# Kernel optimization log

Hardware: AMD Instinct MI355X
Metric: run time of the kernel (lower is better)

## Reference

```python
import jax, jax.numpy as jnp
import numpy as np

B, T_PAST, T_FUT, GH, GW = 256, 20, 30, 100, 100
HID = 32  # past_encoder_dim


def gru_cell(x, h, w_ih, w_hh, b_ih, b_hh):
    # torch nn.GRU single-cell math; weights [3H, in], [3H, H]
    gi = x @ w_ih.T + b_ih
    gh = h @ w_hh.T + b_hh
    i_r, i_z, i_n = jnp.split(gi, 3, axis=-1)
    h_r, h_z, h_n = jnp.split(gh, 3, axis=-1)
    r = jax.nn.sigmoid(i_r + h_r)
    zg = jax.nn.sigmoid(i_z + h_z)
    n = jnp.tanh(i_n + r * h_n)
    return (1.0 - zg) * n + zg * h


def bilinear(grid, q):
    # grid [B,H,W,C]; q [B,2], dim 0 -> height, dim 1 -> width (matches torch code)
    Bn, Hh, Ww, C = grid.shape
    fy = jnp.clip(jnp.floor(q[:, 0]), 0.0, Hh - 2).astype(jnp.int32)
    fx = jnp.clip(jnp.floor(q[:, 1]), 0.0, Ww - 2).astype(jnp.int32)
    ay = jnp.clip(q[:, 0] - fy, 0.0, 1.0)[:, None]
    ax = jnp.clip(q[:, 1] - fx, 0.0, 1.0)[:, None]
    b = jnp.arange(Bn)
    tl = grid[b, fy, fx]
    tr = grid[b, fy, fx + 1]
    bl = grid[b, fy + 1, fx]
    br = grid[b, fy + 1, fx + 1]
    top = tl + ax * (tr - tl)
    bot = bl + ax * (br - bl)
    return top + ay * (bot - top)  # [B,C]


def setup_inputs() -> dict:
    key = jax.random.key(0)
    ks = jax.random.split(key, 24)
    s = 0.05
    f32 = jnp.float32
    inp = {
        'z': jax.random.normal(ks[0], (B, T_FUT, 2), f32),
        'player_past': jax.random.uniform(ks[1], (B, T_PAST, 2), f32) * (GH - 10),
        'lidar': jax.random.normal(ks[2], (B, GH, GW, 2), f32),
        'conv0_w': jax.random.normal(ks[3], (2, 2, 2, 32), f32) * s,   # HWIO
        'conv0_b': jnp.zeros((32,), f32),
        'conv1_w': jax.random.normal(ks[4], (2, 2, 32, 32), f32) * s,
        'conv1_b': jnp.zeros((32,), f32),
        'conv2_w': jax.random.normal(ks[5], (2, 2, 32, 32), f32) * s,
        'conv2_b': jnp.zeros((32,), f32),
        'conv3_w': jax.random.normal(ks[6], (2, 2, 32, 32), f32) * s,
        'conv3_b': jnp.zeros((32,), f32),
        'enc_wih': jax.random.normal(ks[7], (3 * HID, 2), f32) * s,
        'enc_whh': jax.random.normal(ks[8], (3 * HID, HID), f32) * s,
        'enc_bih': jnp.zeros((3 * HID,), f32),
        'enc_bhh': jnp.zeros((3 * HID,), f32),
        'dec_wih': jax.random.normal(ks[9], (3 * HID, HID + 2), f32) * s,
        'dec_whh': jax.random.normal(ks[10], (3 * HID, HID), f32) * s,
        'dec_bih': jnp.zeros((3 * HID,), f32),
        'dec_bhh': jnp.zeros((3 * HID,), f32),
        'mlp_w1': jax.random.normal(ks[11], (512, HID), f32) * s,
        'mlp_b1': jnp.zeros((512,), f32),
        'mlp_w2': jax.random.normal(ks[12], (4, 512), f32) * s,
        'mlp_b2': jnp.zeros((4,), f32),
    }
    return inp


def reference(z, player_past, lidar,
              conv0_w, conv0_b, conv1_w, conv1_b, conv2_w, conv2_b, conv3_w, conv3_b,
              enc_wih, enc_whh, enc_bih, enc_bhh,
              dec_wih, dec_whh, dec_bih, dec_bhh,
              mlp_w1, mlp_b1, mlp_w2, mlp_b2):
    # field model: ZeroPad2d((0,1,0,1)) + Conv 2x2 + ReLU, x4 -> same-size NHWC conv
    v = lidar
    for w, b in ((conv0_w, conv0_b), (conv1_w, conv1_b), (conv2_w, conv2_b), (conv3_w, conv3_b)):
        v = jax.nn.relu(jax.lax.conv_general_dilated(
            v, w, (1, 1), [(0, 1), (0, 1)],
            dimension_numbers=('NHWC', 'HWIO', 'NHWC')) + b)
    context_lidar = v  # [B,GH,GW,32]

    # past encoder GRU; last output of single-layer GRU == final hidden
    h0 = jnp.zeros((z.shape[0], HID), z.dtype)
    def enc_step(h, x_t):
        return gru_cell(x_t, h, enc_wih, enc_whh, enc_bih, enc_bhh), None
    h_enc, _ = jax.lax.scan(enc_step, h0, jnp.swapaxes(player_past, 0, 1))

    y_tm2 = player_past[:, -2, :]
    y_tm1 = player_past[:, -1, :]

    def dec_step(carry, z_t):
        h, y1, y2 = carry
        interp_t = bilinear(context_lidar, y1)                 # [B,32]
        x = jnp.concatenate([y1, interp_t], axis=-1)            # [B,34]
        h = gru_cell(x, h, dec_wih, dec_whh, dec_bih, dec_bhh)
        # locscale_mlp: Linear(32,512) -> Linear(512,4) (no ReLU between, per source)
        ls = (h @ mlp_w1.T + mlp_b1) @ mlp_w2.T + mlp_b2
        loc = ls[:, :2]
        scale = jax.nn.softplus(ls[:, 2:])
        y_t = 2.0 * y1 - y2 + loc + scale * z_t                 # verlet + affine sample
        return (h, y_t, y1), (y_t, scale)

    _, (ys, scales) = jax.lax.scan(dec_step, (h_enc, y_tm1, y_tm2), jnp.swapaxes(z, 0, 1))
    y = jnp.swapaxes(ys, 0, 1)          # [B,T,2]
    scales = jnp.swapaxes(scales, 0, 1)  # [B,T,2]
    logabsdet = jnp.sum(jnp.log(jnp.abs(jnp.prod(scales, axis=-2))), axis=-1)  # [B]
    return (y, logabsdet)
```

## Files before the change

### kernel.cpp

```cpp
#include <hip/hip_runtime.h>
#include <math.h>

typedef __attribute__((ext_vector_type(8))) short    short8;
typedef __attribute__((ext_vector_type(4))) float    f32x4;
typedef __attribute__((ext_vector_type(4))) unsigned uint4v;

#define FRAG0 256

__device__ __forceinline__ unsigned short f2bf(float f) {
    unsigned u = __builtin_bit_cast(unsigned, f);
    u = u + 0x7fffu + ((u >> 16) & 1u);
    return (unsigned short)(u >> 16);
}
__device__ __forceinline__ unsigned packRNE(float hi, float lo) {
    return (unsigned)f2bf(lo) | ((unsigned)f2bf(hi) << 16);
}
__device__ __forceinline__ unsigned pack_trunc(float hi, float lo) {
    return __builtin_amdgcn_perm(__builtin_bit_cast(unsigned, hi),
                                 __builtin_bit_cast(unsigned, lo), 0x07060302u);
}
__device__ __forceinline__ float rfl(float x) {
    return __builtin_bit_cast(float, __builtin_amdgcn_readfirstlane(__builtin_bit_cast(int, x)));
}
__device__ __forceinline__ f32x4 mfma16(short8 a, short8 b, f32x4 c) {
    return __builtin_amdgcn_mfma_f32_16x16x32_bf16(a, b, c, 0, 0, 0);
}
__device__ __forceinline__ unsigned bperm(int addr, unsigned v) {
    return (unsigned)__builtin_amdgcn_ds_bpermute(addr, (int)v);
}
template<int PAT>
__device__ __forceinline__ float swzXf(float v) {
    return __builtin_bit_cast(float, __builtin_amdgcn_ds_swizzle(__builtin_bit_cast(int, v), PAT));
}
__device__ __forceinline__ unsigned swz1u(unsigned v){ return (unsigned)__builtin_amdgcn_ds_swizzle((int)v, 0x041F); }
__device__ __forceinline__ float sigf(float x) { return __builtin_amdgcn_rcpf(1.f + __expf(-x)); }
__device__ __forceinline__ float tanhfast(float x) {
    float e = __expf(2.f * x);
    return 1.f - 2.f * __builtin_amdgcn_rcpf(e + 1.f);
}
__device__ __forceinline__ f32x4 ld4(const float* p) { return *(const f32x4*)p; }

__device__ __forceinline__ void packC(unsigned* P, f32x4 a0, f32x4 a1, bool oob) {
    float r0 = fmaxf(a0[0], 0.f), r1 = fmaxf(a0[1], 0.f), r2 = fmaxf(a0[2], 0.f), r3 = fmaxf(a0[3], 0.f);
    float s0 = fmaxf(a1[0], 0.f), s1 = fmaxf(a1[1], 0.f), s2 = fmaxf(a1[2], 0.f), s3 = fmaxf(a1[3], 0.f);
    P[0] = pack_trunc(r1, r0); P[1] = pack_trunc(r3, r2);
    P[2] = pack_trunc(s1, s0); P[3] = pack_trunc(s3, s2);
    if (oob) { P[0] = 0u; P[1] = 0u; P[2] = 0u; P[3] = 0u; }
}

__global__ __launch_bounds__(256) void r2p2_prep(
    const float* __restrict__ w0, const float* __restrict__ w1,
    const float* __restrict__ w2, const float* __restrict__ w3,
    const float* __restrict__ enc_whh,
    const float* __restrict__ dec_wih, const float* __restrict__ dec_whh,
    const float* __restrict__ mw1, const float* __restrict__ mb1,
    const float* __restrict__ mw2, const float* __restrict__ mb2,
    float* __restrict__ wsf, unsigned* __restrict__ wsu) {
    const int tid = threadIdx.x, bx = blockIdx.x;
    if (bx == 0) {
        __shared__ float red[64];
        if (tid < 128) {
            int k = tid & 31, j = tid >> 5;
            const float* w2r = mw2 + j * 512;
            float a0 = 0.f, a1 = 0.f, a2 = 0.f, a3 = 0.f;
#pragma unroll 4
            for (int m = 0; m < 512; m += 4) {
                a0 = fmaf(w2r[m],     mw1[m * 32 + k],       a0);
                a1 = fmaf(w2r[m + 1], mw1[(m + 1) * 32 + k], a1);
                a2 = fmaf(w2r[m + 2], mw1[(m + 2) * 32 + k], a2);
                a3 = fmaf(w2r[m + 3], mw1[(m + 3) * 32 + k], a3);
            }
            wsf[j * 32 + k] = (a0 + a1) + (a2 + a3);
        } else if (tid < 192) {
            int t = tid - 128;
            int j = t & 3, ch = t >> 2;
            const float* w2c = mw2 + j * 512 + ch * 32;
            const float* b1c = mb1 + ch * 32;
            float p = 0.f;
#pragma unroll 8
            for (int m = 0; m < 32; ++m) p = fmaf(w2c[m], b1c[m], p);
            red[t] = p;
        }
        __syncthreads();
        if (tid < 4) {
            float c = mb2[tid];
#pragma unroll
            for (int i = 0; i < 16; ++i) c += red[tid + i * 4];
            wsf[128 + tid] = c;
        }
        return;
    }
    int base = (bx - 1) * 416;
    for (int c = base + tid; c < base + 416 && c < 2816; c += 256) {
        int f = c >> 6, lane = c & 63;
        int n = lane & 15, q = lane >> 4;
        int pc0 = ((n >> 2) << 3) | (n & 3);
        float v[8];
        if (f < 2) {
            int co = pc0 + f * 4;
#pragma unroll
            for (int j = 0; j < 8; ++j) v[j] = (q == 0) ? w0[j * 32 + co] : 0.f;
        } else if (f < 26) {
            int t = f - 2;
            const float* W = (t < 8) ? w1 : (t < 16) ? w2 : w3;
            t &= 7;
            int mt = t >> 2, ks = t & 3, co = pc0 + mt * 4;
#pragma unroll
            for (int j = 0; j < 8; ++j) v[j] = W[(ks * 32 + q * 8 + j) * 32 + co];
        } else if (f < 32) {
            int t = f - 26, gate = t >> 1, mt = t & 1;
            int row = gate * 32 + pc0 + mt * 4;
#pragma unroll
            for (int j = 0; j < 8; ++j) v[j] = dec_wih[row * 34 + 2 + q * 8 + j];
        } else if (f < 38) {
            int t = f - 32, gate = t >> 1, mt = t & 1;
            int row = gate * 32 + pc0 + mt * 4;
#pragma unroll
            for (int j = 0; j < 8; ++j) v[j] = dec_whh[row * 32 + q * 8 + j];
        } else {
            int t = f - 38, gate = t >> 1, mt = t & 1;
            int row = gate * 32 + pc0 + mt * 4;
#pragma unroll
            for (int j = 0; j < 8; ++j) v[j] = enc_whh[row * 32 + q * 8 + j];
        }
        uint4v u;
        u[0] = packRNE(v[1], v[0]); u[1] = packRNE(v[3], v[2]);
        u[2] = packRNE(v[5], v[4]); u[3] = packRNE(v[7], v[6]);
        *(uint4v*)(wsu + FRAG0 + f * 256 + lane * 4) = u;
    }
}

__global__ __launch_bounds__(256)
void r2p2_main(
    const float* __restrict__ z, const float* __restrict__ past, const float* __restrict__ lidar,
    const float* __restrict__ b0, const float* __restrict__ b1,
    const float* __restrict__ b2, const float* __restrict__ b3,
    const float* __restrict__ enc_wih, const float* __restrict__ enc_bih, const float* __restrict__ enc_bhh,
    const float* __restrict__ dec_wih, const float* __restrict__ dec_bih, const float* __restrict__ dec_bhh,
    const float* __restrict__ wsf, const unsigned* __restrict__ wsu,
    float* __restrict__ out) {

    const int tid = threadIdx.x, b = blockIdx.x;
    const int wid = tid >> 6, lane = tid & 63;
    const int n = lane & 15, q = lane >> 4, e = n & 1;

    __shared__ __align__(16) unsigned sLID[104 * 104];
    __shared__ __align__(16) float PASTs[40];
    __shared__ __align__(16) float ZVs[64];

    if (wid != 0) {
        int st = tid - 64;
        if (st < 60) ZVs[st] = z[b * 60 + st];
        for (int i = st; i < 816; i += 192) {
            int idx = (i < 416) ? (10400 + i) : ((((i - 416) >> 2) * 104) + 100 + ((i - 416) & 3));
            sLID[idx] = 0u;
        }
        const float4* lp4 = (const float4*)(lidar + (size_t)b * 20000);
#pragma unroll 4
        for (int i = st; i < 5000; i += 192) {
            int r = (int)(((unsigned)i * 5243u) >> 18);
            int c2 = i - r * 50;
            float4 v = lp4[i];
            int o = r * 104 + 2 * c2;
            sLID[o]     = pack_trunc(v.y, v.x);
            sLID[o + 1] = pack_trunc(v.w, v.z);
        }
        __syncthreads();
        return;
    }

    uint4v FR[44];
#pragma unroll
    for (int f = 0; f < 44; ++f) FR[f] = *(const uint4v*)(wsu + FRAG0 + f * 256 + lane * 4);
#define FRG(f) __builtin_bit_cast(short8, FR[f])

    f32x4 cb0[2], cb1[2], cb2[2], cb3[2], gbR[2], gbZ[2], gbNi[2], gbNh[2];
    f32x4 egR[2], egZ[2], egNh[2];
#pragma unroll
    for (int mt = 0; mt < 2; ++mt) {
        int o = q * 8 + mt * 4;
        cb0[mt] = ld4(b0 + o); cb1[mt] = ld4(b1 + o); cb2[mt] = ld4(b2 + o); cb3[mt] = ld4(b3 + o);
        gbR[mt]  = ld4(dec_bih + o)      + ld4(dec_bhh + o);
        gbZ[mt]  = ld4(dec_bih + 32 + o) + ld4(dec_bhh + 32 + o);
        gbNi[mt] = ld4(dec_bih + 64 + o);
        gbNh[mt] = ld4(dec_bhh + 64 + o);
        egR[mt]  = ld4(enc_bih + o)      + ld4(enc_bhh + o);
        egZ[mt]  = ld4(enc_bih + 32 + o) + ld4(enc_bhh + 32 + o);
        egNh[mt] = ld4(enc_bhh + 64 + o);
    }
    f32x4 ebni = ld4(enc_bih + 64 + q * 8 + e * 4);
    float2 wxr[4], wxz[4], wxn[4], wexr[4], wexz[4], wexn[4];
#pragma unroll
    for (int r = 0; r < 4; ++r) {
        int c = q * 8 + e * 4 + r;
        wxr[r]  = *(const float2*)(dec_wih + c * 34);
        wxz[r]  = *(const float2*)(dec_wih + (32 + c) * 34);
        wxn[r]  = *(const float2*)(dec_wih + (64 + c) * 34);
        wexr[r] = *(const float2*)(enc_wih + c * 2);
        wexz[r] = *(const float2*)(enc_wih + (32 + c) * 2);
        wexn[r] = *(const float2*)(enc_wih + (64 + c) * 2);
    }
    short8 Am = (short8)0;
    if (n < 4) {
#pragma unroll
        for (int j = 0; j < 8; ++j) Am[j] = (short)f2bf(wsf[n * 32 + q * 8 + j]);
    }
    f32x4 mcv = {0.f, 0.f, 0.f, 0.f};
    if (q == 0) mcv = *(const f32x4*)(wsf + 128);

    if (lane < 20) *(float2*)&PASTs[2 * lane] = *(const float2*)(past + b * 40 + 2 * lane);
    float q0 = past[b * 40 + 38], q1 = past[b * 40 + 39];
    float p0 = past[b * 40 + 36], p1 = past[b * 40 + 37];
    asm volatile("s_waitcnt lgkmcnt(0)" ::: "memory");

    float hq[4] = {0.f, 0.f, 0.f, 0.f};
    short8 hfr = (short8)0;
#pragma unroll 1
    for (int t = 0; t < 20; ++t) {
        float2 xp = *(const float2*)&PASTs[2 * t];
        f32x4 gr0 = mfma16(FRG(38), hfr, egR[0]),  gr1 = mfma16(FRG(39), hfr, egR[1]);
        f32x4 gz0 = mfma16(FRG(40), hfr, egZ[0]),  gz1 = mfma16(FRG(41), hfr, egZ[1]);
        f32x4 gh0 = mfma16(FRG(42), hfr, egNh[0]), gh1 = mfma16(FRG(43), hfr, egNh[1]);
        f32x4 grS = e ? gr1 : gr0, gzS = e ? gz1 : gz0, ghS = e ? gh1 : gh0;
        float hn[4];
#pragma unroll
        for (int r = 0; r < 4; ++r) {
            float rp = grS[r] + xp.x * wexr[r].x + xp.y * wexr[r].y;
            float zp = gzS[r] + xp.x * wexz[r].x + xp.y * wexz[r].y;
            float pi = ebni[r] + xp.x * wexn[r].x + xp.y * wexn[r].y;
            float rr = sigf(rp), zz = sigf(zp);
            float tn = tanhfast(fmaf(rr, ghS[r], pi));
            float hv = tn + zz * (hq[r] - tn);
            hq[r] = hv; hn[r] = hv;
        }
        unsigned hu0 = packRNE(hn[1], hn[0]), hu1 = packRNE(hn[3], hn[2]);
        unsigned po0 = swz1u(hu0), po1 = swz1u(hu1);
        uint4v hv4;
        hv4[0] = e ? po0 : hu0; hv4[1] = e ? po1 : hu1;
        hv4[2] = e ? hu0 : po0; hv4[3] = e ? hu1 : po1;
        hfr = __builtin_bit_cast(short8, hv4);
    }

    __syncthreads();

    int py0a = n / 5, px0a = n % 5;
    int pe0b = (16 + n < 25) ? 16 + n : 24;
    int py0b = pe0b / 5, px0b = pe0b - py0b * 5;
    int ofs0a[4], ofs0b[4];
#pragma unroll
    for (int tp = 0; tp < 4; ++tp) {
        ofs0a[tp] = (py0a + (tp >> 1)) * 104 + px0a + (tp & 1);
        ofs0b[tp] = (py0b + (tp >> 1)) * 104 + px0b + (tp & 1);
    }
    int py1 = n >> 2, px1 = n & 3;
    int adr1[4], sel1m[4];
#pragma unroll
    for (int ks = 0; ks < 4; ++ks) {
        int p = (py1 + (ks >> 1)) * 5 + px1 + (ks & 1);
        adr1[ks] = (q * 16 + (p & 15)) * 4;
        sel1m[ks] = (p >= 16);
    }
    int pe2 = (n < 9) ? n : 8, py2 = pe2 / 3, px2 = pe2 - py2 * 3;
    int adr2[4];
#pragma unroll
    for (int ks = 0; ks < 4; ++ks) adr2[ks] = (q * 16 + (py2 + (ks >> 1)) * 4 + px2 + (ks & 1)) * 4;
    int pe3 = n & 3, py3 = pe3 >> 1, px3 = pe3 & 1;
    int adr3[4];
#pragma unroll
    for (int ks = 0; ks < 4; ++ks) adr3[ks] = (q * 16 + (py3 + (ks >> 1)) * 3 + px3 + (ks & 1)) * 4;
    const f32x4 zf4 = {0.f, 0.f, 0.f, 0.f};
    float la = 0.f;

#pragma unroll 1
    for (int t = 0; t < 30; ++t) {
        float2 zv = *(const float2*)&ZVs[2 * t];
        float f0 = fminf(fmaxf(floorf(q0), 0.f), 98.f);
        float f1v = fminf(fmaxf(floorf(q1), 0.f), 98.f);
        int fy = (int)f0, fx = (int)f1v;
        float ay = fminf(fmaxf(q0 - f0, 0.f), 1.f);
        float ax = fminf(fmaxf(q1 - f1v, 0.f), 1.f);
        int base = fy * 104 + fx;
        int limy = 100 - fy, limx = 100 - fx;

        short8 bfa = (short8)0, bfb = (short8)0;
        if (q == 0) {
            uint4v ua, ub;
#pragma unroll
            for (int tp = 0; tp < 4; ++tp) { ua[tp] = sLID[base + ofs0a[tp]]; ub[tp] = sLID[base + ofs0b[tp]]; }
            bfa = __builtin_bit_cast(short8, ua);
            bfb = __builtin_bit_cast(short8, ub);
        }
        f32x4 ca0 = mfma16(FRG(0), bfa, cb0[0]);
        f32x4 ca1 = mfma16(FRG(1), bfa, cb0[1]);
        f32x4 cB0 = mfma16(FRG(0), bfb, cb0[0]);
        f32x4 cB1 = mfma16(FRG(1), bfb, cb0[1]);
        unsigned Pa[4], Pb[4];
        packC(Pa, ca0, ca1, (py0a >= limy) || (px0a >= limx));
        packC(Pb, cB0, cB1, (py0b >= limy) || (px0b >= limx));

        short8 bf1[4];
#pragma unroll
        for (int ks = 0; ks < 4; ++ks) {
            uint4v bu;
#pragma unroll
            for (int u = 0; u < 4; ++u) {
                unsigned va = bperm(adr1[ks], Pa[u]);
                unsigned vb = bperm(adr1[ks], Pb[u]);
                bu[u] = sel1m[ks] ? vb : va;
            }
            bf1[ks] = __builtin_bit_cast(short8, bu);
        }
        {
            f32x4 aA = mfma16(FRG(2), bf1[0], cb1[0]); aA = mfma16(FRG(3), bf1[1], aA);
            f32x4 aB = mfma16(FRG(4), bf1[2], zf4);    aB = mfma16(FRG(5), bf1[3], aB);
            f32x4 bA = mfma16(FRG(6), bf1[0], cb1[1]); bA = mfma16(FRG(7), bf1[1], bA);
            f32x4 bB = mfma16(FRG(8), bf1[2], zf4);    bB = mfma16(FRG(9), bf1[3], bB);
            f32x4 o0 = aA + aB, o1 = bA + bB;
            packC(Pa, o0, o1, (py1 >= limy) || (px1 >= limx));
        }

        short8 bf2v[4];
#pragma unroll
        for (int ks = 0; ks < 4; ++ks) {
            uint4v bu;
#pragma unroll
            for (int u = 0; u < 4; ++u) bu[u] = bperm(adr2[ks], Pa[u]);
            bf2v[ks] = __builtin_bit_cast(short8, bu);
        }
        {
            f32x4 aA = mfma16(FRG(10), bf2v[0], cb2[0]); aA = mfma16(FRG(11), bf2v[1], aA);
            f32x4 aB = mfma16(FRG(12), bf2v[2], zf4);    aB = mfma16(FRG(13), bf2v[3], aB);
            f32x4 bA = mfma16(FRG(14), bf2v[0], cb2[1]); bA = mfma16(FRG(15), bf2v[1], bA);
            f32x4 bB = mfma16(FRG(16), bf2v[2], zf4);    bB = mfma16(FRG(17), bf2v[3], bB);
            f32x4 o0 = aA + aB, o1 = bA + bB;
            packC(Pb, o0, o1, (py2 >= limy) || (px2 >= limx));
        }

        short8 bf3v[4];
#pragma unroll
        for (int ks = 0; ks < 4; ++ks) {
            uint4v bu;
#pragma unroll
            for (int u = 0; u < 4; ++u) bu[u] = bperm(adr3[ks], Pb[u]);
            bf3v[ks] = __builtin_bit_cast(short8, bu);
        }
        short8 xf;
        {
            f32x4 aA = mfma16(FRG(18), bf3v[0], cb3[0]); aA = mfma16(FRG(19), bf3v[1], aA);
            f32x4 aB = mfma16(FRG(20), bf3v[2], zf4);    aB = mfma16(FRG(21), bf3v[3], aB);
            f32x4 bA = mfma16(FRG(22), bf3v[0], cb3[1]); bA = mfma16(FRG(23), bf3v[1], bA);
            f32x4 bB = mfma16(FRG(24), bf3v[2], zf4);    bB = mfma16(FRG(25), bf3v[3], bB);
            f32x4 o0 = aA + aB, o1 = bA + bB;
            float wy = (n & 2) ? ay : 1.f - ay;
            float wx = (n & 1) ? ax : 1.f - ax;
            float w = wy * wx;
            float t0[4], t1[4];
#pragma unroll
            for (int r = 0; r < 4; ++r) { t0[r] = fmaxf(o0[r], 0.f) * w; t1[r] = fmaxf(o1[r], 0.f) * w; }
#pragma unroll
            for (int r = 0; r < 4; ++r) {
                float a1 = swzXf<0x041F>(t0[r]), a2 = swzXf<0x081F>(t0[r]), a3 = swzXf<0x0C1F>(t0[r]);
                t0[r] = (t0[r] + a1) + (a2 + a3);
                float b1v = swzXf<0x041F>(t1[r]), b2v = swzXf<0x081F>(t1[r]), b3v = swzXf<0x0C1F>(t1[r]);
                t1[r] = (t1[r] + b1v) + (b2v + b3v);
            }
            uint4v xu;
            xu[0] = packRNE(t0[1], t0[0]); xu[1] = packRNE(t0[3], t0[2]);
            xu[2] = packRNE(t1[1], t1[0]); xu[3] = packRNE(t1[3], t1[2]);
            xf = __builtin_bit_cast(short8, xu);
        }

        f32x4 gr0 = mfma16(FRG(26), xf, gbR[0]); gr0 = mfma16(FRG(32), hfr, gr0);
        f32x4 gr1 = mfma16(FRG(27), xf, gbR[1]); gr1 = mfma16(FRG(33), hfr, gr1);
        f32x4 gz0 = mfma16(FRG(28), xf, gbZ[0]); gz0 = mfma16(FRG(34), hfr, gz0);
        f32x4 gz1 = mfma16(FRG(29), xf, gbZ[1]); gz1 = mfma16(FRG(35), hfr, gz1);
        f32x4 gi0 = mfma16(FRG(30), xf, gbNi[0]);
        f32x4 gi1 = mfma16(FRG(31), xf, gbNi[1]);
        f32x4 gh0 = mfma16(FRG(36), hfr, gbNh[0]);
        f32x4 gh1 = mfma16(FRG(37), hfr, gbNh[1]);
        f32x4 grS = e ? gr1 : gr0, gzS = e ? gz1 : gz0, giS = e ? gi1 : gi0, ghS = e ? gh1 : gh0;
        float hn[4];
#pragma unroll
        for (int r = 0; r < 4; ++r) {
            float rp = grS[r] + q0 * wxr[r].x + q1 * wxr[r].y;
            float zp = gzS[r] + q0 * wxz[r].x + q1 * wxz[r].y;
            float pi = giS[r] + q0 * wxn[r].x + q1 * wxn[r].y;
            float rr = sigf(rp), zz = sigf(zp);
            float tn = tanhfast(fmaf(rr, ghS[r], pi));
            float hv = tn + zz * (hq[r] - tn);
            hq[r] = hv; hn[r] = hv;
        }
        unsigned hu0 = packRNE(hn[1], hn[0]), hu1 = packRNE(hn[3], hn[2]);
        unsigned po0 = swz1u(hu0), po1 = swz1u(hu1);
        uint4v hv4;
        hv4[0] = e ? po0 : hu0; hv4[1] = e ? po1 : hu1;
        hv4[2] = e ? hu0 : po0; hv4[3] = e ? hu1 : po1;
        hfr = __builtin_bit_cast(short8, hv4);

        f32x4 ls = mfma16(Am, hfr, mcv);
        float l2 = ls[2], l3 = ls[3];
        float s0 = fmaxf(l2, 0.f) + __logf(1.f + __expf(-fabsf(l2)));
        float s1 = fmaxf(l3, 0.f) + __logf(1.f + __expf(-fabsf(l3)));
        float ny0 = 2.f * q0 - p0 + ls[0] + s0 * zv.x;
        float ny1 = 2.f * q1 - p1 + ls[1] + s1 * zv.y;
        if (lane == 0) {
            float2 o2 = {ny0, ny1};
            *(float2*)(out + b * 60 + 2 * t) = o2;
        }
        la += __logf(s0 * s1);
        p0 = q0; p1 = q1;
        q0 = rfl(ny0); q1 = rfl(ny1);
    }
    if (lane == 0) out[15360 + b] = la;
#undef FRG
}

extern "C" void kernel_launch(void* const* d_in, const int* in_sizes, int n_in,
                              void* d_out, int out_size, void* d_ws, size_t ws_size,
                              hipStream_t stream) {
    const float* z    = (const float*)d_in[0];
    const float* past = (const float*)d_in[1];
    const float* lid  = (const float*)d_in[2];
    const float* c0w = (const float*)d_in[3];  const float* c0b = (const float*)d_in[4];
    const float* c1w = (const float*)d_in[5];  const float* c1b = (const float*)d_in[6];
    const float* c2w = (const float*)d_in[7];  const float* c2b = (const float*)d_in[8];
    const float* c3w = (const float*)d_in[9];  const float* c3b = (const float*)d_in[10];
    const float* ewih = (const float*)d_in[11]; const float* ewhh = (const float*)d_in[12];
    const float* ebih = (const float*)d_in[13]; const float* ebhh = (const float*)d_in[14];
    const float* dwih = (const float*)d_in[15]; const float* dwhh = (const float*)d_in[16];
    const float* dbih = (const float*)d_in[17]; const float* dbhh = (const float*)d_in[18];
    const float* mw1 = (const float*)d_in[19]; const float* mb1 = (const float*)d_in[20];
    const float* mw2 = (const float*)d_in[21]; const float* mb2 = (const float*)d_in[22];
    float* out = (float*)d_out;
    float* wsf = (float*)d_ws;
    unsigned* wsu = (unsigned*)d_ws;

    r2p2_prep<<<8, 256, 0, stream>>>(c0w, c1w, c2w, c3w, ewhh, dwih, dwhh,
                                     mw1, mb1, mw2, mb2, wsf, wsu);
    r2p2_main<<<256, 256, 0, stream>>>(z, past, lid, c0b, c1b, c2b, c3b,
                                       ewih, ebih, ebhh, dwih, dbih, dbhh,
                                       wsf, wsu, out);
}
```

Baseline: 182.4 us.

## Fuse weight-prep kernel into main kernel, packing fragments via shared memory

```diff
diff --git a/kernel.cpp b/kernel.cpp
--- a/kernel.cpp
+++ b/kernel.cpp
@@ -4,8 +4,6 @@
 typedef __attribute__((ext_vector_type(8))) short    short8;
 typedef __attribute__((ext_vector_type(4))) float    f32x4;
 typedef __attribute__((ext_vector_type(4))) unsigned uint4v;
-
-#define FRAG0 256
 
 __device__ __forceinline__ unsigned short f2bf(float f) {
     unsigned u = __builtin_bit_cast(unsigned, f);
@@ -48,107 +46,153 @@
     if (oob) { P[0] = 0u; P[1] = 0u; P[2] = 0u; P[3] = 0u; }
 }
 
-__global__ __launch_bounds__(256) void r2p2_prep(
-    const float* __restrict__ w0, const float* __restrict__ w1,
-    const float* __restrict__ w2, const float* __restrict__ w3,
-    const float* __restrict__ enc_whh,
-    const float* __restrict__ dec_wih, const float* __restrict__ dec_whh,
-    const float* __restrict__ mw1, const float* __restrict__ mb1,
-    const float* __restrict__ mw2, const float* __restrict__ mb2,
-    float* __restrict__ wsf, unsigned* __restrict__ wsu) {
-    const int tid = threadIdx.x, bx = blockIdx.x;
-    if (bx == 0) {
-        __shared__ float red[64];
-        if (tid < 128) {
-            int k = tid & 31, j = tid >> 5;
-            const float* w2r = mw2 + j * 512;
-            float a0 = 0.f, a1 = 0.f, a2 = 0.f, a3 = 0.f;
-#pragma unroll 4
-            for (int m = 0; m < 512; m += 4) {
-                a0 = fmaf(w2r[m],     mw1[m * 32 + k],       a0);
-                a1 = fmaf(w2r[m + 1], mw1[(m + 1) * 32 + k], a1);
-                a2 = fmaf(w2r[m + 2], mw1[(m + 2) * 32 + k], a2);
-                a3 = fmaf(w2r[m + 3], mw1[(m + 3) * 32 + k], a3);
-            }
-            wsf[j * 32 + k] = (a0 + a1) + (a2 + a3);
-        } else if (tid < 192) {
-            int t = tid - 128;
-            int j = t & 3, ch = t >> 2;
-            const float* w2c = mw2 + j * 512 + ch * 32;
-            const float* b1c = mb1 + ch * 32;
-            float p = 0.f;
-#pragma unroll 8
-            for (int m = 0; m < 32; ++m) p = fmaf(w2c[m], b1c[m], p);
-            red[t] = p;
-        }
-        __syncthreads();
-        if (tid < 4) {
-            float c = mb2[tid];
-#pragma unroll
-            for (int i = 0; i < 16; ++i) c += red[tid + i * 4];
-            wsf[128 + tid] = c;
-        }
-        return;
-    }
-    int base = (bx - 1) * 416;
-    for (int c = base + tid; c < base + 416 && c < 2816; c += 256) {
-        int f = c >> 6, lane = c & 63;
-        int n = lane & 15, q = lane >> 4;
-        int pc0 = ((n >> 2) << 3) | (n & 3);
-        float v[8];
-        if (f < 2) {
-            int co = pc0 + f * 4;
-#pragma unroll
-            for (int j = 0; j < 8; ++j) v[j] = (q == 0) ? w0[j * 32 + co] : 0.f;
-        } else if (f < 26) {
-            int t = f - 2;
-            const float* W = (t < 8) ? w1 : (t < 16) ? w2 : w3;
-            t &= 7;
-            int mt = t >> 2, ks = t & 3, co = pc0 + mt * 4;
-#pragma unroll
-            for (int j = 0; j < 8; ++j) v[j] = W[(ks * 32 + q * 8 + j) * 32 + co];
-        } else if (f < 32) {
-            int t = f - 26, gate = t >> 1, mt = t & 1;
-            int row = gate * 32 + pc0 + mt * 4;
-#pragma unroll
-            for (int j = 0; j < 8; ++j) v[j] = dec_wih[row * 34 + 2 + q * 8 + j];
-        } else if (f < 38) {
-            int t = f - 32, gate = t >> 1, mt = t & 1;
-            int row = gate * 32 + pc0 + mt * 4;
-#pragma unroll
-            for (int j = 0; j < 8; ++j) v[j] = dec_whh[row * 32 + q * 8 + j];
-        } else {
-            int t = f - 38, gate = t >> 1, mt = t & 1;
-            int row = gate * 32 + pc0 + mt * 4;
-#pragma unroll
-            for (int j = 0; j < 8; ++j) v[j] = enc_whh[row * 32 + q * 8 + j];
-        }
-        uint4v u;
-        u[0] = packRNE(v[1], v[0]); u[1] = packRNE(v[3], v[2]);
-        u[2] = packRNE(v[5], v[4]); u[3] = packRNE(v[7], v[6]);
-        *(uint4v*)(wsu + FRAG0 + f * 256 + lane * 4) = u;
-    }
+__device__ __forceinline__ uint4v ld4u(const short* p) {
+    const unsigned* u = (const unsigned*)p;
+    uint4v r; r[0] = u[0]; r[1] = u[1]; r[2] = u[2]; r[3] = u[3];
+    return r;
 }
 
 __global__ __launch_bounds__(256)
 void r2p2_main(
     const float* __restrict__ z, const float* __restrict__ past, const float* __restrict__ lidar,
-    const float* __restrict__ b0, const float* __restrict__ b1,
-    const float* __restrict__ b2, const float* __restrict__ b3,
-    const float* __restrict__ enc_wih, const float* __restrict__ enc_bih, const float* __restrict__ enc_bhh,
-    const float* __restrict__ dec_wih, const float* __restrict__ dec_bih, const float* __restrict__ dec_bhh,
-    const float* __restrict__ wsf, const unsigned* __restrict__ wsu,
+    const float* __restrict__ w0, const float* __restrict__ b0,
+    const float* __restrict__ w1, const float* __restrict__ b1,
+    const float* __restrict__ w2, const float* __restrict__ b2,
+    const float* __restrict__ w3, const float* __restrict__ b3,
+    const float* __restrict__ enc_wih, const float* __restrict__ enc_whh,
+    const float* __restrict__ enc_bih, const float* __restrict__ enc_bhh,
+    const float* __restrict__ dec_wih, const float* __restrict__ dec_whh,
+    const float* __restrict__ dec_bih, const float* __restrict__ dec_bhh,
+    const float* __restrict__ mw1, const float* __restrict__ mb1,
+    const float* __restrict__ mw2, const float* __restrict__ mb2,
     float* __restrict__ out) {
 
     const int tid = threadIdx.x, b = blockIdx.x;
     const int wid = tid >> 6, lane = tid & 63;
     const int n = lane & 15, q = lane >> 4, e = n & 1;
-
-    __shared__ __align__(16) unsigned sLID[104 * 104];
+    const int pc0 = ((n >> 2) << 3) | (n & 3);
+
+    __shared__ __align__(16) unsigned sLID[10816];
+    __shared__ __align__(16) short sG[9792];
     __shared__ __align__(16) float PASTs[40];
     __shared__ __align__(16) float ZVs[64];
-
-    if (wid != 0) {
+    __shared__ __align__(16) float MMs[132];
+
+    short* sW = (short*)sLID;
+
+    for (int i = tid; i < 4096; i += 256) {
+        int k = i >> 5, co = i & 31;
+        sW[          co * 130 + k] = (short)f2bf(w1[i]);
+        sW[4160 +    co * 130 + k] = (short)f2bf(w2[i]);
+        sW[8320 +    co * 130 + k] = (short)f2bf(w3[i]);
+    }
+    for (int i = tid; i < 3072; i += 256) {
+        int o = i >> 5, k = i & 31;
+        sG[       o * 34 + k] = (short)f2bf(dec_wih[o * 34 + 2 + k]);
+        sG[3264 + o * 34 + k] = (short)f2bf(dec_whh[i]);
+        sG[6528 + o * 34 + k] = (short)f2bf(enc_whh[i]);
+    }
+    __syncthreads();
+
+    uint4v FR[44];
+    f32x4 cb0[2], cb1[2], cb2[2], cb3[2], gbR[2], gbZ[2], gbNi[2], gbNh[2];
+    f32x4 egR[2], egZ[2], egNh[2], ebni = {0.f, 0.f, 0.f, 0.f};
+    float2 wxr[4], wxz[4], wxn[4], wexr[4], wexz[4], wexn[4];
+    float q0 = 0.f, q1 = 0.f, p0 = 0.f, p1 = 0.f;
+
+    if (wid == 0) {
+        if (q == 0) {
+#pragma unroll
+            for (int mt = 0; mt < 2; ++mt) {
+                int co = pc0 + mt * 4;
+                uint4v u;
+#pragma unroll
+                for (int i = 0; i < 4; ++i) u[i] = packRNE(w0[(2 * i + 1) * 32 + co], w0[2 * i * 32 + co]);
+                FR[mt] = u;
+            }
+        } else { FR[0] = (uint4v)0u; FR[1] = (uint4v)0u; }
+#pragma unroll
+        for (int mt = 0; mt < 2; ++mt) {
+            int co = pc0 + mt * 4;
+#pragma unroll
+            for (int ks = 0; ks < 4; ++ks) {
+                FR[ 2 + mt * 4 + ks] = ld4u(sW +        co * 130 + ks * 32 + q * 8);
+                FR[10 + mt * 4 + ks] = ld4u(sW + 4160 + co * 130 + ks * 32 + q * 8);
+                FR[18 + mt * 4 + ks] = ld4u(sW + 8320 + co * 130 + ks * 32 + q * 8);
+            }
+        }
+#pragma unroll
+        for (int g = 0; g < 3; ++g) {
+#pragma unroll
+            for (int mt = 0; mt < 2; ++mt) {
+                int o = (g * 32 + pc0 + mt * 4) * 34 + q * 8;
+                FR[26 + g * 2 + mt] = ld4u(sG + o);
+                FR[32 + g * 2 + mt] = ld4u(sG + 3264 + o);
+                FR[38 + g * 2 + mt] = ld4u(sG + 6528 + o);
+            }
+        }
+#pragma unroll
+        for (int mt = 0; mt < 2; ++mt) {
+            int o = q * 8 + mt * 4;
+            cb0[mt] = ld4(b0 + o); cb1[mt] = ld4(b1 + o); cb2[mt] = ld4(b2 + o); cb3[mt] = ld4(b3 + o);
+            gbR[mt]  = ld4(dec_bih + o)      + ld4(dec_bhh + o);
+            gbZ[mt]  = ld4(dec_bih + 32 + o) + ld4(dec_bhh + 32 + o);
+            gbNi[mt] = ld4(dec_bih + 64 + o);
+            gbNh[mt] = ld4(dec_bhh + 64 + o);
+            egR[mt]  = ld4(enc_bih + o)      + ld4(enc_bhh + o);
+            egZ[mt]  = ld4(enc_bih + 32 + o) + ld4(enc_bhh + 32 + o);
+            egNh[mt] = ld4(enc_bhh + 64 + o);
+        }
+        ebni = ld4(enc_bih + 64 + q * 8 + e * 4);
+#pragma unroll
+        for (int r = 0; r < 4; ++r) {
+            int c = q * 8 + e * 4 + r;
+            wxr[r]  = *(const float2*)(dec_wih + c * 34);
+            wxz[r]  = *(const float2*)(dec_wih + (32 + c) * 34);
+            wxn[r]  = *(const float2*)(dec_wih + (64 + c) * 34);
+            wexr[r] = *(const float2*)(enc_wih + c * 2);
+            wexz[r] = *(const float2*)(enc_wih + (32 + c) * 2);
+            wexn[r] = *(const float2*)(enc_wih + (64 + c) * 2);
+        }
+        if (lane < 20) *(float2*)&PASTs[2 * lane] = *(const float2*)(past + b * 40 + 2 * lane);
+        q0 = past[b * 40 + 38]; q1 = past[b * 40 + 39];
+        p0 = past[b * 40 + 36]; p1 = past[b * 40 + 37];
+    }
+    __syncthreads();
+
+#define FRG(f) __builtin_bit_cast(short8, FR[f])
+
+    float hq[4] = {0.f, 0.f, 0.f, 0.f};
+    short8 hfr = (short8)0;
+
+    if (wid == 0) {
+        asm volatile("s_waitcnt lgkmcnt(0)" ::: "memory");
+#pragma unroll 1
+        for (int t = 0; t < 20; ++t) {
+            float2 xp = *(const float2*)&PASTs[2 * t];
+            f32x4 gr0 = mfma16(FRG(38), hfr, egR[0]),  gr1 = mfma16(FRG(39), hfr, egR[1]);
+            f32x4 gz0 = mfma16(FRG(40), hfr, egZ[0]),  gz1 = mfma16(FRG(41), hfr, egZ[1]);
+            f32x4 gh0 = mfma16(FRG(42), hfr, egNh[0]), gh1 = mfma16(FRG(43), hfr, egNh[1]);
+            f32x4 grS = e ? gr1 : gr0, gzS = e ? gz1 : gz0, ghS = e ? gh1 : gh0;
+            float hn[4];
+#pragma unroll
+            for (int r = 0; r < 4; ++r) {
+                float rp = grS[r] + xp.x * wexr[r].x + xp.y * wexr[r].y;
+                float zp = gzS[r] + xp.x * wexz[r].x + xp.y * wexz[r].y;
+                float pi = ebni[r] + xp.x * wexn[r].x + xp.y * wexn[r].y;
+                float rr = sigf(rp), zz = sigf(zp);
+                float tn = tanhfast(fmaf(rr, ghS[r], pi));
+                float hv = tn + zz * (hq[r] - tn);
+                hq[r] = hv; hn[r] = hv;
+            }
+            unsigned hu0 = packRNE(hn[1], hn[0]), hu1 = packRNE(hn[3], hn[2]);
+            unsigned po0 = swz1u(hu0), po1 = swz1u(hu1);
+            uint4v hv4;
+            hv4[0] = e ? po0 : hu0; hv4[1] = e ? po1 : hu1;
+            hv4[2] = e ? hu0 : po0; hv4[3] = e ? hu1 : po1;
+            hfr = __builtin_bit_cast(short8, hv4);
+        }
+    } else {
         int st = tid - 64;
         if (st < 60) ZVs[st] = z[b * 60 + st];
         for (int i = st; i < 816; i += 192) {
@@ -165,83 +209,43 @@
             sLID[o]     = pack_trunc(v.y, v.x);
             sLID[o + 1] = pack_trunc(v.w, v.z);
         }
-        __syncthreads();
-        return;
-    }
-
-    uint4v FR[44];
-#pragma unroll
-    for (int f = 0; f < 44; ++f) FR[f] = *(const uint4v*)(wsu + FRAG0 + f * 256 + lane * 4);
-#define FRG(f) __builtin_bit_cast(short8, FR[f])
-
-    f32x4 cb0[2], cb1[2], cb2[2], cb3[2], gbR[2], gbZ[2], gbNi[2], gbNh[2];
-    f32x4 egR[2], egZ[2], egNh[2];
-#pragma unroll
-    for (int mt = 0; mt < 2; ++mt) {
-        int o = q * 8 + mt * 4;
-        cb0[mt] = ld4(b0 + o); cb1[mt] = ld4(b1 + o); cb2[mt] = ld4(b2 + o); cb3[mt] = ld4(b3 + o);
-        gbR[mt]  = ld4(dec_bih + o)      + ld4(dec_bhh + o);
-        gbZ[mt]  = ld4(dec_bih + 32 + o) + ld4(dec_bhh + 32 + o);
-        gbNi[mt] = ld4(dec_bih + 64 + o);
-        gbNh[mt] = ld4(dec_bhh + 64 + o);
-        egR[mt]  = ld4(enc_bih + o)      + ld4(enc_bhh + o);
-        egZ[mt]  = ld4(enc_bih + 32 + o) + ld4(enc_bhh + 32 + o);
-        egNh[mt] = ld4(enc_bhh + 64 + o);
-    }
-    f32x4 ebni = ld4(enc_bih + 64 + q * 8 + e * 4);
-    float2 wxr[4], wxz[4], wxn[4], wexr[4], wexz[4], wexn[4];
-#pragma unroll
-    for (int r = 0; r < 4; ++r) {
-        int c = q * 8 + e * 4 + r;
-        wxr[r]  = *(const float2*)(dec_wih + c * 34);
-        wxz[r]  = *(const float2*)(dec_wih + (32 + c) * 34);
-        wxn[r]  = *(const float2*)(dec_wih + (64 + c) * 34);
-        wexr[r] = *(const float2*)(enc_wih + c * 2);
-        wexz[r] = *(const float2*)(enc_wih + (32 + c) * 2);
-        wexn[r] = *(const float2*)(enc_wih + (64 + c) * 2);
-    }
+        if (wid < 3) {
+            int o = tid - 64;
+            int j = o >> 5, k = o & 31;
+            const float* w2r = mw2 + j * 512;
+            float a0 = 0.f, a1 = 0.f, a2 = 0.f, a3 = 0.f;
+#pragma unroll 4
+            for (int m = 0; m < 512; m += 4) {
+                a0 = fmaf(w2r[m],     mw1[m * 32 + k],       a0);
+                a1 = fmaf(w2r[m + 1], mw1[(m + 1) * 32 + k], a1);
+                a2 = fmaf(w2r[m + 2], mw1[(m + 2) * 32 + k], a2);
+                a3 = fmaf(w2r[m + 3], mw1[(m + 3) * 32 + k], a3);
+            }
+            MMs[j * 32 + k] = (a0 + a1) + (a2 + a3);
+        } else {
+            int j = lane & 3, ch = lane >> 2;
+            const float* w2c = mw2 + j * 512 + ch * 32;
+            const float* b1c = mb1 + ch * 32;
+            float p = 0.f;
+#pragma unroll 8
+            for (int m = 0; m < 32; ++m) p = fmaf(w2c[m], b1c[m], p);
+            p += __shfl_xor(p, 4, 64);
+            p += __shfl_xor(p, 8, 64);
+            p += __shfl_xor(p, 16, 64);
+            p += __shfl_xor(p, 32, 64);
+            if (lane < 4) MMs[128 + lane] = p + mb2[lane];
+        }
+    }
+    __syncthreads();
+    if (wid != 0) return;
+
     short8 Am = (short8)0;
     if (n < 4) {
 #pragma unroll
-        for (int j = 0; j < 8; ++j) Am[j] = (short)f2bf(wsf[n * 32 + q * 8 + j]);
+        for (int j = 0; j < 8; ++j) Am[j] = (short)f2bf(MMs[n * 32 + q * 8 + j]);
     }
     f32x4 mcv = {0.f, 0.f, 0.f, 0.f};
-    if (q == 0) mcv = *(const f32x4*)(wsf + 128);
-
-    if (lane < 20) *(float2*)&PASTs[2 * lane] = *(const float2*)(past + b * 40 + 2 * lane);
-    float q0 = past[b * 40 + 38], q1 = past[b * 40 + 39];
-    float p0 = past[b * 40 + 36], p1 = past[b * 40 + 37];
-    asm volatile("s_waitcnt lgkmcnt(0)" ::: "memory");
-
-    float hq[4] = {0.f, 0.f, 0.f, 0.f};
-    short8 hfr = (short8)0;
-#pragma unroll 1
-    for (int t = 0; t < 20; ++t) {
-        float2 xp = *(const float2*)&PASTs[2 * t];
-        f32x4 gr0 = mfma16(FRG(38), hfr, egR[0]),  gr1 = mfma16(FRG(39), hfr, egR[1]);
-        f32x4 gz0 = mfma16(FRG(40), hfr, egZ[0]),  gz1 = mfma16(FRG(41), hfr, egZ[1]);
-        f32x4 gh0 = mfma16(FRG(42), hfr, egNh[0]), gh1 = mfma16(FRG(43), hfr, egNh[1]);
-        f32x4 grS = e ? gr1 : gr0, gzS = e ? gz1 : gz0, ghS = e ? gh1 : gh0;
-        float hn[4];
-#pragma unroll
-        for (int r = 0; r < 4; ++r) {
-            float rp = grS[r] + xp.x * wexr[r].x + xp.y * wexr[r].y;
-            float zp = gzS[r] + xp.x * wexz[r].x + xp.y * wexz[r].y;
-            float pi = ebni[r] + xp.x * wexn[r].x + xp.y * wexn[r].y;
-            float rr = sigf(rp), zz = sigf(zp);
-            float tn = tanhfast(fmaf(rr, ghS[r], pi));
-            float hv = tn + zz * (hq[r] - tn);
-            hq[r] = hv; hn[r] = hv;
-        }
-        unsigned hu0 = packRNE(hn[1], hn[0]), hu1 = packRNE(hn[3], hn[2]);
-        unsigned po0 = swz1u(hu0), po1 = swz1u(hu1);
-        uint4v hv4;
-        hv4[0] = e ? po0 : hu0; hv4[1] = e ? po1 : hu1;
-        hv4[2] = e ? hu0 : po0; hv4[3] = e ? hu1 : po1;
-        hfr = __builtin_bit_cast(short8, hv4);
-    }
-
-    __syncthreads();
+    if (q == 0) mcv = *(const f32x4*)(MMs + 128);
 
     int py0a = n / 5, px0a = n % 5;
     int pe0b = (16 + n < 25) ? 16 + n : 24;
@@ -432,12 +436,10 @@
     const float* mw1 = (const float*)d_in[19]; const float* mb1 = (const float*)d_in[20];
     const float* mw2 = (const float*)d_in[21]; const float* mb2 = (const float*)d_in[22];
     float* out = (float*)d_out;
-    float* wsf = (float*)d_ws;
-    unsigned* wsu = (unsigned*)d_ws;
-
-    r2p2_prep<<<8, 256, 0, stream>>>(c0w, c1w, c2w, c3w, ewhh, dwih, dwhh,
-                                     mw1, mb1, mw2, mb2, wsf, wsu);
-    r2p2_main<<<256, 256, 0, stream>>>(z, past, lid, c0b, c1b, c2b, c3b,
-                                       ewih, ebih, ebhh, dwih, dbih, dbhh,
-                                       wsf, wsu, out);
-}
+
+    r2p2_main<<<256, 256, 0, stream>>>(z, past, lid,
+                                       c0w, c0b, c1w, c1b, c2w, c2b, c3w, c3b,
+                                       ewih, ewhh, ebih, ebhh,
+                                       dwih, dwhh, dbih, dbhh,
+                                       mw1, mb1, mw2, mb2, out);
+}
```

Measured after the change: 207.8 us. +13.9%, slower.
